# Optimization experiments

Hardware: AMD Instinct MI355X
Metric: run time of the kernel (lower is better)

Reference implementation:

```python
import jax, jax.numpy as jnp
import numpy as np

B, N, K, C = 4, 4096, 32, 192  # batch, npoint, nsample, channels (C % 6 == 0)
EPS = 1e-5


def setup_inputs() -> dict:
    key = jax.random.key(0)
    ks = jax.random.split(key, 8)
    p = jax.random.normal(ks[0], (B, N, 3), jnp.float32)
    x = jax.random.normal(ks[1], (B, C, N), jnp.float32)
    idx = jax.random.randint(ks[2], (B, N, K), 0, N)  # ball-query neighbor ids
    W = jax.random.normal(ks[3], (C, C + 3), jnp.float32) * 0.05  # 1x1 conv weight
    gamma = 1.0 + 0.1 * jax.random.normal(ks[4], (C,), jnp.float32)
    beta = 0.1 * jax.random.normal(ks[5], (C,), jnp.float32)
    rmean = 0.1 * jax.random.normal(ks[6], (C,), jnp.float32)
    rvar = jax.random.uniform(ks[7], (C,), jnp.float32) + 0.5  # positive running var
    return dict(p=p, x=x, idx=idx, W=W, gamma=gamma, beta=beta, rmean=rmean, rvar=rvar)


def reference(p, x, idx, W, gamma, beta, rmean, rvar):
    # --- grouper: gather neighbors, relative coords ---
    pn = jax.vmap(lambda pp, ii: pp[ii])(p, idx)            # [B,N,K,3]
    dp = jnp.transpose(pn - p[:, :, None, :], (0, 3, 1, 2))  # [B,3,N,K]
    xj = jax.vmap(lambda xx, ii: xx[:, ii])(x, idx)          # [B,C,N,K]
    # --- PosPool sin/cos positional embedding fused with features ---
    feat_dim = C // 6
    dim_mat = jnp.power(500.0, jnp.arange(feat_dim, dtype=jnp.float32) / feat_dim)
    div = (50.0 * dp)[..., None] / dim_mat                   # [B,3,N,K,fd]
    pe = jnp.concatenate([jnp.sin(div), jnp.cos(div)], axis=-1)  # [B,3,N,K,2fd]
    pe = jnp.transpose(pe, (0, 1, 4, 2, 3)).reshape(B, C, N, K)  # [B,C,N,K]
    agg = xj * pe + pe
    # --- dp_fj concat -> 1x1 conv -> BN(eval) -> ReLU ---
    h = jnp.concatenate([dp, agg], axis=1)                   # [B,C+3,N,K]
    y = jnp.einsum('oc,bcnk->bonk', W, h)                    # [B,C,N,K]
    inv = gamma / jnp.sqrt(rvar + EPS)
    y = y * inv[:, None, None] + (beta - rmean * inv)[:, None, None]
    y = jax.nn.relu(y)
    # --- max reduction over neighbors ---
    return jnp.max(y, axis=-1)                               # [B,C,N]
```

## Files before the change

kernel.cpp:

```cpp
#include <hip/hip_runtime.h>
#include <math.h>

#define B_   4
#define N_   4096
#define K_   32
#define C_   192
#define CH_  195
#define KPAD 224
#define PTS  2
#define NKT  7
#define NNT  4
#define GRID ((B_ * N_) / PTS)

using half8  = __attribute__((ext_vector_type(8))) _Float16;
using half2v = __attribute__((ext_vector_type(2))) _Float16;
using f32x4  = __attribute__((ext_vector_type(4))) float;

__device__ _Float16 g_Wp[C_ * KPAD];
__device__ _Float16 g_xT[(size_t)B_ * N_ * C_];

__device__ __forceinline__ float dpp_max16(float v) {
    int s;
    s = __builtin_amdgcn_update_dpp(0, __float_as_int(v), 0xB1,  0xF, 0xF, true);
    v = fmaxf(v, __int_as_float(s));
    s = __builtin_amdgcn_update_dpp(0, __float_as_int(v), 0x4E,  0xF, 0xF, true);
    v = fmaxf(v, __int_as_float(s));
    s = __builtin_amdgcn_update_dpp(0, __float_as_int(v), 0x141, 0xF, 0xF, true);
    v = fmaxf(v, __int_as_float(s));
    s = __builtin_amdgcn_update_dpp(0, __float_as_int(v), 0x140, 0xF, 0xF, true);
    v = fmaxf(v, __int_as_float(s));
    return v;
}

__global__ __launch_bounds__(256) void prep_w(const float* __restrict__ W) {
    int i = blockIdx.x * 256 + threadIdx.x;
    if (i < C_ * KPAD) {
        int o = i / KPAD, r = i - o * KPAD;
        float v = 0.0f;
        if (r < 3)                  v = W[o * CH_ + r];
        else if (r >= 8 && r < 200) v = W[o * CH_ + 3 + (r - 8)];
        g_Wp[i] = (_Float16)v;
    }
}

__global__ __launch_bounds__(256) void prep_xt(const float* __restrict__ x) {
    __shared__ float s[32][97];
    const int tid = threadIdx.x;
    const int b   = blockIdx.z;
    const int c0  = blockIdx.y * 96;
    const int n0  = blockIdx.x * 32;
#pragma unroll
    for (int it = 0; it < 3; ++it) {
        const int c  = it * 32 + (tid >> 3);
        const int n4 = (tid & 7) * 4;
        const float4 v = *(const float4*)(x + ((size_t)b * C_ + c0 + c) * N_ + n0 + n4);
        s[n4 + 0][c] = v.x; s[n4 + 1][c] = v.y; s[n4 + 2][c] = v.z; s[n4 + 3][c] = v.w;
    }
    __syncthreads();
#pragma unroll
    for (int it = 0; it < 2; ++it) {
        const int t = it * 256 + tid;
        if (t < 32 * 12) {
            const int n  = t / 12;
            const int ch = t - n * 12;
            half8 v;
#pragma unroll
            for (int jj = 0; jj < 8; ++jj) v[jj] = (_Float16)s[n][ch * 8 + jj];
            *(half8*)(g_xT + ((size_t)b * N_ + n0 + n) * C_ + c0 + ch * 8) = v;
        }
    }
}

__global__ __launch_bounds__(256, 4) void la_mfma(
    const float* __restrict__ p,
    const int*   __restrict__ idx,
    const float* __restrict__ gamma_,
    const float* __restrict__ beta_,
    const float* __restrict__ rmean,
    const float* __restrict__ rvar,
    float* __restrict__ out)
{
    __shared__ _Float16 hb[NKT * NNT * 64 * 8];
    __shared__ float s_inv[C_], s_bias[C_], s_fr[32];

    const int tid  = threadIdx.x;
    const int lane = tid & 63;
    const int w    = tid >> 6;

    const int q  = blockIdx.x & 7;
    const int sI = blockIdx.x >> 3;
    const int L  = q * (GRID / 8) + sI;
    const int bn0 = L * PTS;
    const int b   = bn0 >> 12;
    const int n0  = bn0 & (N_ - 1);

    if (tid < C_) {
        const float inv = gamma_[tid] * rsqrtf(rvar[tid] + 1e-5f);
        s_inv[tid]  = inv;
        s_bias[tid] = beta_[tid] - rmean[tid] * inv;
    }
    if (tid < 32) s_fr[tid] = 7.9577471546e0f * exp2f(-(float)tid * 0.2801808715263400f);
    __syncthreads();

    {
        const int lsl = lane & 15;
        const int q0  = lane >> 4;
        const int col = w * 16 + lsl;
        const int pt  = col >> 5;
        const int k   = col & 31;
        const int gp  = bn0 + pt;
        const int j   = idx[(size_t)gp * K_ + k];
        const float d0 = p[(size_t)(b * N_ + j) * 3 + 0] - p[(size_t)gp * 3 + 0];
        const float d1 = p[(size_t)(b * N_ + j) * 3 + 1] - p[(size_t)gp * 3 + 1];
        const float d2 = p[(size_t)(b * N_ + j) * 3 + 2] - p[(size_t)gp * 3 + 2];
        const _Float16* xh = g_xT + ((size_t)b * N_ + j) * C_;

        float sfr[8];
#pragma unroll
        for (int jj = 0; jj < 8; ++jj) sfr[jj] = s_fr[q0 * 8 + jj];

#pragma unroll
        for (int i = 0; i < 6; ++i) {
            const int chunk = q0 + 4 * i;
            const half8 v = *(const half8*)(xh + chunk * 8);
            const float dd  = (chunk < 8) ? d0 : ((chunk < 16) ? d1 : d2);
            const float off = (chunk & 4) ? 0.25f : 0.0f;
            half8 hv;
#pragma unroll
            for (int jj = 0; jj < 8; jj += 2) {
                const float pe0 = __builtin_amdgcn_sinf(fmaf(dd, sfr[jj],     off));
                const float pe1 = __builtin_amdgcn_sinf(fmaf(dd, sfr[jj + 1], off));
                const half2v pe2 = __builtin_bit_cast(half2v, __builtin_amdgcn_cvt_pkrtz(pe0, pe1));
                half2v v2; v2[0] = v[jj]; v2[1] = v[jj + 1];
                const half2v r2 = pe2 * v2 + pe2;
                hv[jj] = r2[0]; hv[jj + 1] = r2[1];
            }
            const int ro = chunk + 1;
            const int kt = ro >> 2, kq = ro & 3;
            *(half8*)(&hb[(size_t)((kt * NNT + w) * 64 + kq * 16 + lsl) * 8]) = hv;
        }
        if (q0 == 0) {
            half8 hv0 = (half8)(_Float16)0.0f;
            hv0[0] = (_Float16)d0; hv0[1] = (_Float16)d1; hv0[2] = (_Float16)d2;
            *(half8*)(&hb[(size_t)((0 * NNT + w) * 64 + 0 * 16 + lsl) * 8]) = hv0;
        } else {
            const int ro = 24 + q0;
            const int kt = ro >> 2, kq = ro & 3;
            *(half8*)(&hb[(size_t)((kt * NNT + w) * 64 + kq * 16 + lsl) * 8]) = (half8)(_Float16)0.0f;
        }
    }
    __syncthreads();

    const int l15  = lane & 15;
    const int quad = lane >> 4;

    f32x4 acc[3][4];
#pragma unroll
    for (int i = 0; i < 3; ++i)
#pragma unroll
        for (int t = 0; t < 4; ++t) acc[i][t] = (f32x4)0.0f;

#pragma unroll
    for (int kt = 0; kt < 7; ++kt) {
        const int k0 = kt * 32 + quad * 8;
        half8 a[3], bf[4];
#pragma unroll
        for (int i = 0; i < 3; ++i) {
            const int m = (w * 3 + i) * 16 + l15;
            a[i] = *(const half8*)(g_Wp + (size_t)m * KPAD + k0);
        }
#pragma unroll
        for (int t = 0; t < 4; ++t)
            bf[t] = *(const half8*)(&hb[(size_t)((kt * NNT + t) * 64 + lane) * 8]);
#pragma unroll
        for (int i = 0; i < 3; ++i)
#pragma unroll
            for (int t = 0; t < 4; ++t)
                acc[i][t] = __builtin_amdgcn_mfma_f32_16x16x32_f16(a[i], bf[t], acc[i][t], 0, 0, 0);
    }

    __syncthreads();
    float* s_out = (float*)hb;

#pragma unroll
    for (int i = 0; i < 3; ++i) {
        const int mbase = (w * 3 + i) * 16 + quad * 4;
#pragma unroll
        for (int pt = 0; pt < PTS; ++pt) {
            const f32x4 va = acc[i][2 * pt];
            const f32x4 vb = acc[i][2 * pt + 1];
#pragma unroll
            for (int r = 0; r < 4; ++r) {
                const int m = mbase + r;
                const float inv = s_inv[m];
                const float bia = s_bias[m];
                float v = fmaxf(fmaf(va[r], inv, bia), fmaf(vb[r], inv, bia));
                v = dpp_max16(v);
                if (l15 == 0) s_out[m * PTS + pt] = fmaxf(v, 0.0f);
            }
        }
    }
    __syncthreads();

    if (tid < C_) {
        const float2 o2 = *(const float2*)(&s_out[tid * PTS]);
        *(float2*)(&out[((size_t)b * C_ + tid) * N_ + n0]) = o2;
    }
}

extern "C" void kernel_launch(void* const* d_in, const int* in_sizes, int n_in,
                              void* d_out, int out_size, void* d_ws, size_t ws_size,
                              hipStream_t stream) {
    (void)in_sizes; (void)n_in; (void)out_size; (void)d_ws; (void)ws_size;
    const float* p      = (const float*)d_in[0];
    const float* x      = (const float*)d_in[1];
    const int*   idx    = (const int*)d_in[2];
    const float* W      = (const float*)d_in[3];
    const float* gamma_ = (const float*)d_in[4];
    const float* beta_  = (const float*)d_in[5];
    const float* rmean  = (const float*)d_in[6];
    const float* rvar   = (const float*)d_in[7];
    float* out = (float*)d_out;

    prep_w<<<(C_ * KPAD + 255) / 256, 256, 0, stream>>>(W);
    prep_xt<<<dim3(N_ / 32, 2, B_), 256, 0, stream>>>(x);
    la_mfma<<<GRID, 256, 0, stream>>>(p, idx, gamma_, beta_, rmean, rvar, out);
}
```

Before: 173.0 us.

## Make main kernel persistent with register-resident weights and fold BN scale into W

The main kernel becomes persistent: a fixed grid of 768 blocks loops over point groups, still split by XCD. Each wave now loads its slice of the f16 weight matrix into registers once, instead of re-reading it from global memory for every group. The BN scale is folded into the weights during prep, so the epilogue takes the max first and adds the bias only after the DPP reduction. The two prep kernels are merged into one launch. The trade-off is more register pressure (launch bounds drop from 4 to 3 waves) and an extra sync per loop iteration; folding the scale before the f16 cast also changes rounding slightly.

```diff
diff --git a/kernel.cpp b/kernel.cpp
--- a/kernel.cpp
+++ b/kernel.cpp
@@ -10,7 +10,10 @@
 #define PTS  2
 #define NKT  7
 #define NNT  4
-#define GRID ((B_ * N_) / PTS)
+#define NGROUPS ((B_ * N_) / PTS)
+#define GPX  (NGROUPS / 8)
+#define BPX  96
+#define GRID (8 * BPX)
 
 using half8  = __attribute__((ext_vector_type(8))) _Float16;
 using half2v = __attribute__((ext_vector_type(2))) _Float16;
@@ -32,46 +35,51 @@
     return v;
 }
 
-__global__ __launch_bounds__(256) void prep_w(const float* __restrict__ W) {
-    int i = blockIdx.x * 256 + threadIdx.x;
-    if (i < C_ * KPAD) {
-        int o = i / KPAD, r = i - o * KPAD;
-        float v = 0.0f;
-        if (r < 3)                  v = W[o * CH_ + r];
-        else if (r >= 8 && r < 200) v = W[o * CH_ + 3 + (r - 8)];
-        g_Wp[i] = (_Float16)v;
-    }
-}
-
-__global__ __launch_bounds__(256) void prep_xt(const float* __restrict__ x) {
+__global__ __launch_bounds__(256) void prep(const float* __restrict__ x,
+                                            const float* __restrict__ W,
+                                            const float* __restrict__ gamma_,
+                                            const float* __restrict__ rvar) {
     __shared__ float s[32][97];
     const int tid = threadIdx.x;
-    const int b   = blockIdx.z;
-    const int c0  = blockIdx.y * 96;
-    const int n0  = blockIdx.x * 32;
-#pragma unroll
-    for (int it = 0; it < 3; ++it) {
-        const int c  = it * 32 + (tid >> 3);
-        const int n4 = (tid & 7) * 4;
-        const float4 v = *(const float4*)(x + ((size_t)b * C_ + c0 + c) * N_ + n0 + n4);
-        s[n4 + 0][c] = v.x; s[n4 + 1][c] = v.y; s[n4 + 2][c] = v.z; s[n4 + 3][c] = v.w;
-    }
-    __syncthreads();
-#pragma unroll
-    for (int it = 0; it < 2; ++it) {
-        const int t = it * 256 + tid;
-        if (t < 32 * 12) {
-            const int n  = t / 12;
-            const int ch = t - n * 12;
-            half8 v;
-#pragma unroll
-            for (int jj = 0; jj < 8; ++jj) v[jj] = (_Float16)s[n][ch * 8 + jj];
-            *(half8*)(g_xT + ((size_t)b * N_ + n0 + n) * C_ + c0 + ch * 8) = v;
-        }
-    }
-}
-
-__global__ __launch_bounds__(256, 4) void la_mfma(
+    if (blockIdx.x < 1024) {
+        const int bi = blockIdx.x;
+        const int b  = bi >> 8;
+        const int c0 = ((bi >> 7) & 1) * 96;
+        const int n0 = (bi & 127) * 32;
+#pragma unroll
+        for (int it = 0; it < 3; ++it) {
+            const int c  = it * 32 + (tid >> 3);
+            const int n4 = (tid & 7) * 4;
+            const float4 v = *(const float4*)(x + ((size_t)b * C_ + c0 + c) * N_ + n0 + n4);
+            s[n4 + 0][c] = v.x; s[n4 + 1][c] = v.y; s[n4 + 2][c] = v.z; s[n4 + 3][c] = v.w;
+        }
+        __syncthreads();
+#pragma unroll
+        for (int it = 0; it < 2; ++it) {
+            const int t = it * 256 + tid;
+            if (t < 32 * 12) {
+                const int n  = t / 12;
+                const int ch = t - n * 12;
+                half8 v;
+#pragma unroll
+                for (int jj = 0; jj < 8; ++jj) v[jj] = (_Float16)s[n][ch * 8 + jj];
+                *(half8*)(g_xT + ((size_t)b * N_ + n0 + n) * C_ + c0 + ch * 8) = v;
+            }
+        }
+    } else {
+        const int i = (blockIdx.x - 1024) * 256 + tid;
+        if (i < C_ * KPAD) {
+            const int o = i / KPAD, r = i - o * KPAD;
+            const float inv = gamma_[o] * rsqrtf(rvar[o] + 1e-5f);
+            float v = 0.0f;
+            if (r < 3)                  v = W[o * CH_ + r];
+            else if (r >= 8 && r < 200) v = W[o * CH_ + 3 + (r - 8)];
+            g_Wp[i] = (_Float16)(v * inv);
+        }
+    }
+}
+
+__global__ __launch_bounds__(256, 3) void la_mfma(
     const float* __restrict__ p,
     const int*   __restrict__ idx,
     const float* __restrict__ gamma_,
@@ -81,130 +89,130 @@
     float* __restrict__ out)
 {
     __shared__ _Float16 hb[NKT * NNT * 64 * 8];
-    __shared__ float s_inv[C_], s_bias[C_], s_fr[32];
+    __shared__ float s_bias[C_], s_fr[32], s_out[C_ * PTS];
 
     const int tid  = threadIdx.x;
     const int lane = tid & 63;
     const int w    = tid >> 6;
-
-    const int q  = blockIdx.x & 7;
-    const int sI = blockIdx.x >> 3;
-    const int L  = q * (GRID / 8) + sI;
-    const int bn0 = L * PTS;
-    const int b   = bn0 >> 12;
-    const int n0  = bn0 & (N_ - 1);
+    const int l15  = lane & 15;
+    const int quad = lane >> 4;
 
     if (tid < C_) {
         const float inv = gamma_[tid] * rsqrtf(rvar[tid] + 1e-5f);
-        s_inv[tid]  = inv;
         s_bias[tid] = beta_[tid] - rmean[tid] * inv;
     }
-    if (tid < 32) s_fr[tid] = 7.9577471546e0f * exp2f(-(float)tid * 0.2801808715263400f);
+    if (tid < 32) s_fr[tid] = 7.9577471546f * exp2f(-(float)tid * 0.2801808715263400f);
+
+    half8 areg[3][NKT];
+#pragma unroll
+    for (int i = 0; i < 3; ++i) {
+        const int m = (w * 3 + i) * 16 + l15;
+#pragma unroll
+        for (int kt = 0; kt < NKT; ++kt)
+            areg[i][kt] = *(const half8*)(g_Wp + (size_t)m * KPAD + kt * 32 + quad * 8);
+    }
     __syncthreads();
 
-    {
-        const int lsl = lane & 15;
-        const int q0  = lane >> 4;
-        const int col = w * 16 + lsl;
-        const int pt  = col >> 5;
-        const int k   = col & 31;
-        const int gp  = bn0 + pt;
-        const int j   = idx[(size_t)gp * K_ + k];
-        const float d0 = p[(size_t)(b * N_ + j) * 3 + 0] - p[(size_t)gp * 3 + 0];
-        const float d1 = p[(size_t)(b * N_ + j) * 3 + 1] - p[(size_t)gp * 3 + 1];
-        const float d2 = p[(size_t)(b * N_ + j) * 3 + 2] - p[(size_t)gp * 3 + 2];
-        const _Float16* xh = g_xT + ((size_t)b * N_ + j) * C_;
-
-        float sfr[8];
-#pragma unroll
-        for (int jj = 0; jj < 8; ++jj) sfr[jj] = s_fr[q0 * 8 + jj];
-
-#pragma unroll
-        for (int i = 0; i < 6; ++i) {
-            const int chunk = q0 + 4 * i;
-            const half8 v = *(const half8*)(xh + chunk * 8);
-            const float dd  = (chunk < 8) ? d0 : ((chunk < 16) ? d1 : d2);
-            const float off = (chunk & 4) ? 0.25f : 0.0f;
-            half8 hv;
-#pragma unroll
-            for (int jj = 0; jj < 8; jj += 2) {
-                const float pe0 = __builtin_amdgcn_sinf(fmaf(dd, sfr[jj],     off));
-                const float pe1 = __builtin_amdgcn_sinf(fmaf(dd, sfr[jj + 1], off));
-                const half2v pe2 = __builtin_bit_cast(half2v, __builtin_amdgcn_cvt_pkrtz(pe0, pe1));
-                half2v v2; v2[0] = v[jj]; v2[1] = v[jj + 1];
-                const half2v r2 = pe2 * v2 + pe2;
-                hv[jj] = r2[0]; hv[jj + 1] = r2[1];
-            }
-            const int ro = chunk + 1;
-            const int kt = ro >> 2, kq = ro & 3;
-            *(half8*)(&hb[(size_t)((kt * NNT + w) * 64 + kq * 16 + lsl) * 8]) = hv;
-        }
-        if (q0 == 0) {
-            half8 hv0 = (half8)(_Float16)0.0f;
-            hv0[0] = (_Float16)d0; hv0[1] = (_Float16)d1; hv0[2] = (_Float16)d2;
-            *(half8*)(&hb[(size_t)((0 * NNT + w) * 64 + 0 * 16 + lsl) * 8]) = hv0;
-        } else {
-            const int ro = 24 + q0;
-            const int kt = ro >> 2, kq = ro & 3;
-            *(half8*)(&hb[(size_t)((kt * NNT + w) * 64 + kq * 16 + lsl) * 8]) = (half8)(_Float16)0.0f;
-        }
-    }
-    __syncthreads();
-
-    const int l15  = lane & 15;
-    const int quad = lane >> 4;
-
-    f32x4 acc[3][4];
-#pragma unroll
-    for (int i = 0; i < 3; ++i)
-#pragma unroll
-        for (int t = 0; t < 4; ++t) acc[i][t] = (f32x4)0.0f;
-
-#pragma unroll
-    for (int kt = 0; kt < 7; ++kt) {
-        const int k0 = kt * 32 + quad * 8;
-        half8 a[3], bf[4];
+    float sfr[8];
+#pragma unroll
+    for (int jj = 0; jj < 8; ++jj) sfr[jj] = s_fr[quad * 8 + jj];
+
+    const int xcd = blockIdx.x & 7;
+    const int loc = blockIdx.x >> 3;
+    const int colB = w * 16 + l15;
+    const int ptB  = colB >> 5;
+    const int kB   = colB & 31;
+
+    for (int gl = loc; gl < GPX; gl += BPX) {
+        const int grp = xcd * GPX + gl;
+        const int bn0 = grp * PTS;
+        const int b   = bn0 >> 12;
+        const int n0  = bn0 & (N_ - 1);
+
+        {
+            const int gp = bn0 + ptB;
+            const int j  = idx[(size_t)gp * K_ + kB];
+            const float d0 = p[(size_t)(b * N_ + j) * 3 + 0] - p[(size_t)gp * 3 + 0];
+            const float d1 = p[(size_t)(b * N_ + j) * 3 + 1] - p[(size_t)gp * 3 + 1];
+            const float d2 = p[(size_t)(b * N_ + j) * 3 + 2] - p[(size_t)gp * 3 + 2];
+            const _Float16* xh = g_xT + ((size_t)b * N_ + j) * C_;
+
+#pragma unroll
+            for (int i6 = 0; i6 < 6; ++i6) {
+                const int chunk = quad + 4 * i6;
+                const half8 v = *(const half8*)(xh + chunk * 8);
+                const float dd  = (chunk < 8) ? d0 : ((chunk < 16) ? d1 : d2);
+                const float off = (chunk & 4) ? 0.25f : 0.0f;
+                half8 hv;
+#pragma unroll
+                for (int jj = 0; jj < 8; jj += 2) {
+                    const float pe0 = __builtin_amdgcn_sinf(fmaf(dd, sfr[jj],     off));
+                    const float pe1 = __builtin_amdgcn_sinf(fmaf(dd, sfr[jj + 1], off));
+                    const half2v pe2 = __builtin_bit_cast(half2v, __builtin_amdgcn_cvt_pkrtz(pe0, pe1));
+                    half2v v2; v2[0] = v[jj]; v2[1] = v[jj + 1];
+                    const half2v r2 = pe2 * v2 + pe2;
+                    hv[jj] = r2[0]; hv[jj + 1] = r2[1];
+                }
+                const int ro = chunk + 1;
+                const int kt = ro >> 2, kq = ro & 3;
+                *(half8*)(&hb[(size_t)((kt * NNT + w) * 64 + kq * 16 + l15) * 8]) = hv;
+            }
+            if (quad == 0) {
+                half8 hv0 = (half8)(_Float16)0.0f;
+                hv0[0] = (_Float16)d0; hv0[1] = (_Float16)d1; hv0[2] = (_Float16)d2;
+                *(half8*)(&hb[(size_t)((0 * NNT + w) * 64 + 0 * 16 + l15) * 8]) = hv0;
+            } else {
+                const int ro = 24 + quad;
+                const int kt = ro >> 2, kq = ro & 3;
+                *(half8*)(&hb[(size_t)((kt * NNT + w) * 64 + kq * 16 + l15) * 8]) = (half8)(_Float16)0.0f;
+            }
+        }
+        __syncthreads();
+
+        f32x4 acc[3][4];
+#pragma unroll
+        for (int i = 0; i < 3; ++i)
+#pragma unroll
+            for (int t = 0; t < 4; ++t) acc[i][t] = (f32x4)0.0f;
+
+#pragma unroll
+        for (int kt = 0; kt < NKT; ++kt) {
+            half8 bf[4];
+#pragma unroll
+            for (int t = 0; t < 4; ++t)
+                bf[t] = *(const half8*)(&hb[(size_t)((kt * NNT + t) * 64 + lane) * 8]);
+#pragma unroll
+            for (int i = 0; i < 3; ++i)
+#pragma unroll
+                for (int t = 0; t < 4; ++t)
+                    acc[i][t] = __builtin_amdgcn_mfma_f32_16x16x32_f16(areg[i][kt], bf[t], acc[i][t], 0, 0, 0);
+        }
+        __syncthreads();
+
 #pragma unroll
         for (int i = 0; i < 3; ++i) {
-            const int m = (w * 3 + i) * 16 + l15;
-            a[i] = *(const half8*)(g_Wp + (size_t)m * KPAD + k0);
-        }
-#pragma unroll
-        for (int t = 0; t < 4; ++t)
-            bf[t] = *(const half8*)(&hb[(size_t)((kt * NNT + t) * 64 + lane) * 8]);
-#pragma unroll
-        for (int i = 0; i < 3; ++i)
-#pragma unroll
-            for (int t = 0; t < 4; ++t)
-                acc[i][t] = __builtin_amdgcn_mfma_f32_16x16x32_f16(a[i], bf[t], acc[i][t], 0, 0, 0);
-    }
-
-    __syncthreads();
-    float* s_out = (float*)hb;
-
-#pragma unroll
-    for (int i = 0; i < 3; ++i) {
-        const int mbase = (w * 3 + i) * 16 + quad * 4;
-#pragma unroll
-        for (int pt = 0; pt < PTS; ++pt) {
-            const f32x4 va = acc[i][2 * pt];
-            const f32x4 vb = acc[i][2 * pt + 1];
-#pragma unroll
-            for (int r = 0; r < 4; ++r) {
-                const int m = mbase + r;
-                const float inv = s_inv[m];
-                const float bia = s_bias[m];
-                float v = fmaxf(fmaf(va[r], inv, bia), fmaf(vb[r], inv, bia));
-                v = dpp_max16(v);
-                if (l15 == 0) s_out[m * PTS + pt] = fmaxf(v, 0.0f);
-            }
-        }
-    }
-    __syncthreads();
-
-    if (tid < C_) {
-        const float2 o2 = *(const float2*)(&s_out[tid * PTS]);
-        *(float2*)(&out[((size_t)b * C_ + tid) * N_ + n0]) = o2;
+            const int mbase = (w * 3 + i) * 16 + quad * 4;
+#pragma unroll
+            for (int pt = 0; pt < PTS; ++pt) {
+                const f32x4 va = acc[i][2 * pt];
+                const f32x4 vb = acc[i][2 * pt + 1];
+#pragma unroll
+                for (int r = 0; r < 4; ++r) {
+                    float v = fmaxf(va[r], vb[r]);
+                    v = dpp_max16(v);
+                    if (l15 == 0) {
+                        const int m = mbase + r;
+                        s_out[m * PTS + pt] = fmaxf(v + s_bias[m], 0.0f);
+                    }
+                }
+            }
+        }
+        __syncthreads();
+
+        if (tid < C_) {
+            const float2 o2 = *(const float2*)(&s_out[tid * PTS]);
+            *(float2*)(&out[((size_t)b * C_ + tid) * N_ + n0]) = o2;
+        }
     }
 }
 
@@ -222,7 +230,6 @@
     const float* rvar   = (const float*)d_in[7];
     float* out = (float*)d_out;
 
-    prep_w<<<(C_ * KPAD + 255) / 256, 256, 0, stream>>>(W);
-    prep_xt<<<dim3(N_ / 32, 2, B_), 256, 0, stream>>>(x);
+    prep<<<1024 + (C_ * KPAD + 255) / 256, 256, 0, stream>>>(x, W, gamma_, rvar);
     la_mfma<<<GRID, 256, 0, stream>>>(p, idx, gamma_, beta_, rmean, rvar, out);
 }
```

Result: slower. 234.6 us (+35.6%).
